# Kernel optimization log

Measured on AMD Instinct MI355X. Metric: run time of the kernel, lower is better.

Reference implementation:

```python
import jax, jax.numpy as jnp
import numpy as np

NUM_HEADS = 8
SCALE = 25.0
SIM_THRESH = 0.75


def setup_inputs() -> dict:
    key = jax.random.key(0)
    k1, k2, k3, k4 = jax.random.split(key, 4)
    B, N, C = 1, 2048, 1024
    x_cls = jax.random.normal(k1, (B, N, C), jnp.float32)
    cls_score = jax.random.uniform(k2, (N,), jnp.float32)
    fg_score = jax.random.uniform(k3, (N,), jnp.float32)
    W_qkv = jax.random.normal(k4, (3 * C, C), jnp.float32) * 0.02
    return {"x_cls": x_cls, "cls_score": cls_score, "fg_score": fg_score, "W_qkv": W_qkv}


def reference(x_cls, cls_score, fg_score, W_qkv):
    B, N, C = x_cls.shape
    H = NUM_HEADS
    hd = C // H
    # qkv projection (Linear without bias): [B,N,3C] -> [3,B,H,N,hd]
    qkv = (x_cls @ W_qkv.T).reshape(B, N, 3, H, hd).transpose(2, 0, 3, 1, 4)
    q, k, v = qkv[0], qkv[1], qkv[2]
    # cosine normalization
    qn = q / jnp.linalg.norm(q, axis=-1, keepdims=True)
    kn = k / jnp.linalg.norm(k, axis=-1, keepdims=True)
    vn = v / jnp.linalg.norm(v, axis=-1, keepdims=True)
    # cls_score broadcast to [1,1,1,N] (columns); fg_score is unused downstream
    cs = cls_score.reshape(1, 1, 1, N)
    # raw v-v similarity map [B,H,N,N]
    attn_cls_raw = vn @ jnp.swapaxes(vn, -2, -1)
    # use_mask=True path: mask[i,j] = cls_score[j] > cls_score[i] - 0.1
    cs_mask = (cs > jnp.swapaxes(cs, -2, -1) - 0.1).astype(x_cls.dtype)
    # scaled, score-weighted, masked attention; dropout p=0 is identity
    attn = jax.nn.softmax((qn @ jnp.swapaxes(kn, -2, -1)) * SCALE * cs * cs_mask, axis=-1)
    x = jnp.swapaxes(attn @ v, 1, 2).reshape(B, N, C)
    x_ori = jnp.swapaxes(v, 1, 2).reshape(B, N, C)
    x_out = jnp.concatenate([x, x_ori], axis=-1)  # [B,N,2C]
    # ave=True branch: head-averaged similarity + second softmax, masked renorm
    sim_raw = attn_cls_raw.sum(axis=1)[0] / H  # [N,N]
    sim_mask = (sim_raw > SIM_THRESH).astype(x_cls.dtype)
    sim_attn = attn.sum(axis=1)[0] / H
    sim_round2 = jax.nn.softmax(sim_attn, axis=-1)
    masked = sim_mask * sim_round2
    sim_round2 = masked / jnp.sum(masked, axis=-1, keepdims=True)
    return (x_out, sim_round2)
```

## Files before the change

### kernel.cpp

```cpp
#include <hip/hip_runtime.h>
#include <cstdint>

typedef unsigned short u16;
typedef __attribute__((ext_vector_type(8))) short short8;
typedef __attribute__((ext_vector_type(4))) short short4v;
typedef __attribute__((ext_vector_type(4))) float f32x4;

#define NTOK 2048
#define CDIM 1024
#define C3   3072
#define NH   8
#define HD   128

__device__ __forceinline__ float bf2f(u16 u) {
    return __uint_as_float(((unsigned)u) << 16);
}
__device__ __forceinline__ u16 f2bf(float f) {
    unsigned u = __float_as_uint(f);
    u += 0x7fffu + ((u >> 16) & 1u);
    return (u16)(u >> 16);
}
__device__ __forceinline__ void gld_lds16(const u16* g, u16* l) {
    __builtin_amdgcn_global_load_lds(
        (__attribute__((address_space(1))) void*)(u16*)g,
        (__attribute__((address_space(3))) void*)l, 16, 0, 0);
}

__global__ __launch_bounds__(256) void k_cast(const float* __restrict__ x,
                                              const float* __restrict__ w,
                                              u16* __restrict__ xb,
                                              u16* __restrict__ wb) {
    int t = blockIdx.x * blockDim.x + threadIdx.x;
    int stride = gridDim.x * blockDim.x;
    for (int i = t; i < (NTOK * CDIM) / 4; i += stride) {
        float4 v = ((const float4*)x)[i];
        ushort4 o;
        o.x = f2bf(v.x); o.y = f2bf(v.y); o.z = f2bf(v.z); o.w = f2bf(v.w);
        ((ushort4*)xb)[i] = o;
    }
    for (int i = t; i < (C3 * CDIM) / 4; i += stride) {
        float4 v = ((const float4*)w)[i];
        ushort4 o;
        o.x = f2bf(v.x); o.y = f2bf(v.y); o.z = f2bf(v.z); o.w = f2bf(v.w);
        ((ushort4*)wb)[i] = o;
    }
}

__global__ __launch_bounds__(256) void k_qkvn(const u16* __restrict__ A,
                                              const u16* __restrict__ B,
                                              u16* __restrict__ Qn,
                                              u16* __restrict__ Kn,
                                              u16* __restrict__ Vn,
                                              u16* __restrict__ Vt,
                                              float* __restrict__ out) {
    __shared__ u16 lds[128 * 136];
    __shared__ float rowssq[128][2];
    u16* As = lds;
    u16* Bs = lds + 128 * 64;
    const int tid = threadIdx.x;
    const int lane = tid & 63;
    const int wid = tid >> 6;
    const int wm = wid >> 1, wn = wid & 1;
    const int q = lane >> 4, l16 = lane & 15;
    const int s = blockIdx.x;
    const int which = s >> 3, h = s & 7;
    const int m0 = blockIdx.y * 128, n0 = s * 128;

    f32x4 zero4 = {0.f, 0.f, 0.f, 0.f};
    f32x4 acc[4][4];
#pragma unroll
    for (int i = 0; i < 4; i++)
#pragma unroll
        for (int j = 0; j < 4; j++) acc[i][j] = zero4;

    const u16* aP[4];
    const u16* bP[4];
#pragma unroll
    for (int t = 0; t < 4; t++) {
        int sl = tid + t * 256;
        int r = sl >> 3, c = (sl & 7) * 8;
        aP[t] = &A[(long long)(m0 + r) * CDIM + c];
        bP[t] = &B[(long long)(n0 + r) * CDIM + c];
    }

    for (int k0 = 0; k0 < CDIM; k0 += 64) {
        __syncthreads();
#pragma unroll
        for (int t = 0; t < 4; t++) {
            int sl = tid + t * 256;
            gld_lds16(aP[t] + k0, &As[sl * 8]);
            gld_lds16(bP[t] + k0, &Bs[sl * 8]);
        }
        __syncthreads();
#pragma unroll
        for (int ks = 0; ks < 2; ks++) {
            short8 af[4], bfr[4];
#pragma unroll
            for (int tm = 0; tm < 4; tm++)
                af[tm] = *(const short8*)&As[(wm * 64 + tm * 16 + l16) * 64 + ks * 32 + q * 8];
#pragma unroll
            for (int tn = 0; tn < 4; tn++)
                bfr[tn] = *(const short8*)&Bs[(wn * 64 + tn * 16 + l16) * 64 + ks * 32 + q * 8];
#pragma unroll
            for (int tm = 0; tm < 4; tm++)
#pragma unroll
                for (int tn = 0; tn < 4; tn++)
                    acc[tm][tn] = __builtin_amdgcn_mfma_f32_16x16x32_bf16(
                        af[tm], bfr[tn], acc[tm][tn], 0, 0, 0);
        }
    }

    __syncthreads();
#pragma unroll
    for (int tm = 0; tm < 4; tm++)
#pragma unroll
        for (int r = 0; r < 4; r++) {
            float p = 0.f;
#pragma unroll
            for (int tn = 0; tn < 4; tn++) p += acc[tm][tn][r] * acc[tm][tn][r];
            p += __shfl_xor(p, 1);
            p += __shfl_xor(p, 2);
            p += __shfl_xor(p, 4);
            p += __shfl_xor(p, 8);
            if (l16 == 0) rowssq[wm * 64 + tm * 16 + q * 4 + r][wn] = p;
        }
    __syncthreads();
    float rinv[4][4];
#pragma unroll
    for (int tm = 0; tm < 4; tm++)
#pragma unroll
        for (int r = 0; r < 4; r++) {
            int rl = wm * 64 + tm * 16 + q * 4 + r;
            rinv[tm][r] = rsqrtf(rowssq[rl][0] + rowssq[rl][1]);
        }
    u16* dstBase = (which == 0 ? Qn : which == 1 ? Kn : Vn);
#pragma unroll
    for (int tm = 0; tm < 4; tm++)
#pragma unroll
        for (int tn = 0; tn < 4; tn++)
#pragma unroll
            for (int r = 0; r < 4; r++) {
                int rl = wm * 64 + tm * 16 + q * 4 + r;
                int d = wn * 64 + tn * 16 + l16;
                dstBase[(long long)(m0 + rl) * CDIM + h * HD + d] =
                    f2bf(acc[tm][tn][r] * rinv[tm][r]);
            }
    if (which == 2) {
#pragma unroll
        for (int tm = 0; tm < 4; tm++)
#pragma unroll
            for (int tn = 0; tn < 4; tn++)
#pragma unroll
                for (int r = 0; r < 4; r++) {
                    int rl = wm * 64 + tm * 16 + q * 4 + r;
                    int d = wn * 64 + tn * 16 + l16;
                    float v = acc[tm][tn][r];
                    out[(long long)(m0 + rl) * 2048 + 1024 + h * HD + d] = v;
                    lds[rl * 136 + d] = f2bf(v);
                }
        __syncthreads();
#pragma unroll
        for (int p = 0; p < 2; p++) {
            int drow = p * 64 + (tid >> 2);
            int nc = (tid & 3) * 32;
            u16 buf[32];
#pragma unroll
            for (int i = 0; i < 32; i++) buf[i] = lds[(nc + i) * 136 + drow];
            u16* dst = &Vt[(long long)(h * HD + drow) * NTOK + m0 + nc];
            *(short8*)&dst[0] = *(short8*)&buf[0];
            *(short8*)&dst[8] = *(short8*)&buf[8];
            *(short8*)&dst[16] = *(short8*)&buf[16];
            *(short8*)&dst[24] = *(short8*)&buf[24];
        }
    }
}

__global__ __launch_bounds__(256) void k_gemm_mask(const u16* __restrict__ A,
                                                   const u16* __restrict__ B,
                                                   unsigned char* __restrict__ Cv,
                                                   int K, int lda, int ldb, int ldc,
                                                   float scale) {
    if (blockIdx.x > blockIdx.y) return;
    __shared__ u16 As[128 * 64];
    __shared__ u16 Bs[128 * 64];
    __shared__ __attribute__((aligned(16))) unsigned char Tm[128][144];
    __shared__ __attribute__((aligned(16))) unsigned char Tt[128][144];
    const int tid = threadIdx.x;
    const int lane = tid & 63;
    const int wid = tid >> 6;
    const int wm = wid >> 1, wn = wid & 1;
    const int q = lane >> 4, l16 = lane & 15;
    const int m0 = blockIdx.y * 128, n0 = blockIdx.x * 128;

    f32x4 zero4 = {0.f, 0.f, 0.f, 0.f};
    f32x4 acc[4][4];
#pragma unroll
    for (int i = 0; i < 4; i++)
#pragma unroll
        for (int j = 0; j < 4; j++) acc[i][j] = zero4;

    const u16* aP[4];
    const u16* bP[4];
#pragma unroll
    for (int t = 0; t < 4; t++) {
        int s = tid + t * 256;
        int r = s >> 3, c = (s & 7) * 8;
        aP[t] = &A[(long long)(m0 + r) * lda + c];
        bP[t] = &B[(long long)(n0 + r) * ldb + c];
    }

    for (int k0 = 0; k0 < K; k0 += 64) {
        __syncthreads();
#pragma unroll
        for (int t = 0; t < 4; t++) {
            int s = tid + t * 256;
            gld_lds16(aP[t] + k0, &As[s * 8]);
            gld_lds16(bP[t] + k0, &Bs[s * 8]);
        }
        __syncthreads();
#pragma unroll
        for (int ks = 0; ks < 2; ks++) {
            short8 af[4], bfr[4];
#pragma unroll
            for (int tm = 0; tm < 4; tm++)
                af[tm] = *(const short8*)&As[(wm * 64 + tm * 16 + l16) * 64 + ks * 32 + q * 8];
#pragma unroll
            for (int tn = 0; tn < 4; tn++)
                bfr[tn] = *(const short8*)&Bs[(wn * 64 + tn * 16 + l16) * 64 + ks * 32 + q * 8];
#pragma unroll
            for (int tm = 0; tm < 4; tm++)
#pragma unroll
                for (int tn = 0; tn < 4; tn++)
                    acc[tm][tn] = __builtin_amdgcn_mfma_f32_16x16x32_bf16(
                        af[tm], bfr[tn], acc[tm][tn], 0, 0, 0);
        }
    }

#pragma unroll
    for (int tm = 0; tm < 4; tm++)
#pragma unroll
        for (int tn = 0; tn < 4; tn++) {
            int col = wn * 64 + tn * 16 + l16;
            int rowbase = wm * 64 + tm * 16 + q * 4;
            unsigned pack = 0;
#pragma unroll
            for (int r = 0; r < 4; r++) {
                unsigned char b = (acc[tm][tn][r] * scale > 0.75f) ? 1 : 0;
                Tm[rowbase + r][col] = b;
                pack |= ((unsigned)b) << (8 * r);
            }
            *(unsigned*)&Tt[col][rowbase] = pack;
        }
    __syncthreads();
    {
        int row = tid >> 1, half = (tid & 1) * 64;
        const short8* sm = (const short8*)&Tm[row][half];
        short8* dm = (short8*)&Cv[(long long)(m0 + row) * ldc + n0 + half];
        dm[0] = sm[0]; dm[1] = sm[1]; dm[2] = sm[2]; dm[3] = sm[3];
        const short8* st = (const short8*)&Tt[row][half];
        short8* dt = (short8*)&Cv[(long long)(n0 + row) * ldc + m0 + half];
        dt[0] = st[0]; dt[1] = st[1]; dt[2] = st[2]; dt[3] = st[3];
    }
}

__global__ __launch_bounds__(256, 4) void k_attn8(const u16* __restrict__ Qn,
                                                  const u16* __restrict__ Kn,
                                                  const u16* __restrict__ Vt,
                                                  const float* __restrict__ cls,
                                                  u16* __restrict__ P,
                                                  float* __restrict__ Spart,
                                                  u16* __restrict__ Xpart) {
    __shared__ u16 Kf[2][8192];
    __shared__ u16 Vf[2][8192];
    __shared__ u16 Et[4096];
    const int h = blockIdx.z;
    const int jc = blockIdx.y;
    const int i0 = blockIdx.x * 64;
    const int jbase = jc * 512;
    const int tid = threadIdx.x, lane = tid & 63, wid = tid >> 6;
    const int q = lane >> 4, l16 = lane & 15;
    const int wm = wid >> 1, wn = wid & 1;

    short8 af[2][4];
#pragma unroll
    for (int m = 0; m < 2; m++)
#pragma unroll
        for (int kt = 0; kt < 4; kt++)
            af[m][kt] = *(const short8*)&Qn[(long long)(i0 + wm * 32 + m * 16 + l16) * CDIM +
                                            h * HD + kt * 32 + q * 8];
    float cls_i[2][4];
#pragma unroll
    for (int m = 0; m < 2; m++)
#pragma unroll
        for (int r = 0; r < 4; r++)
            cls_i[m][r] = cls[i0 + wm * 32 + m * 16 + q * 4 + r] - 0.1f;

    const u16* ksrc[4];
    const u16* vsrc[4];
#pragma unroll
    for (int t = 0; t < 4; t++) {
        int g = wid * 4 + t;
        int tn = g >> 2, kt = g & 3;
        ksrc[t] = &Kn[(long long)(jbase + tn * 16 + l16) * CDIM + h * HD + kt * 32 + q * 8];
        int n = g >> 1, ks = g & 1;
        vsrc[t] = &Vt[(long long)(h * HD + n * 16 + l16) * NTOK + jbase + (ks * 4 + q) * 8];
    }

    f32x4 zero4 = {0.f, 0.f, 0.f, 0.f};
    f32x4 pv[2][4];
#pragma unroll
    for (int m = 0; m < 2; m++)
#pragma unroll
        for (int n = 0; n < 4; n++) pv[m][n] = zero4;
    float sums[2][4] = {{0.f, 0.f, 0.f, 0.f}, {0.f, 0.f, 0.f, 0.f}};

#pragma unroll
    for (int t = 0; t < 4; t++) {
        int g = wid * 4 + t;
        gld_lds16(ksrc[t], &Kf[0][(g * 64 + lane) * 8]);
        gld_lds16(vsrc[t], &Vf[0][(g * 64 + lane) * 8]);
        ksrc[t] += 64 * CDIM;
        vsrc[t] += 64;
    }

    for (int jt = 0; jt < 8; ++jt) {
        const int j0 = jbase + jt * 64;
        const int cur = jt & 1;
        u16* Kc = Kf[cur];
        u16* Vc = Vf[cur];
        if (jt == 0)
            asm volatile("s_waitcnt vmcnt(0)" ::: "memory");
        else
            asm volatile("s_waitcnt vmcnt(2)" ::: "memory");
        __builtin_amdgcn_s_barrier();
        asm volatile("" ::: "memory");
        if (jt < 7) {
            u16* Kx = Kf[cur ^ 1];
            u16* Vx = Vf[cur ^ 1];
#pragma unroll
            for (int t = 0; t < 4; t++) {
                int g = wid * 4 + t;
                gld_lds16(ksrc[t], &Kx[(g * 64 + lane) * 8]);
                gld_lds16(vsrc[t], &Vx[(g * 64 + lane) * 8]);
                ksrc[t] += 64 * CDIM;
                vsrc[t] += 64;
            }
        }
#pragma unroll
        for (int tn = 0; tn < 2; tn++) {
            int tng = wn * 2 + tn;
            short8 bfr[4];
#pragma unroll
            for (int kt = 0; kt < 4; kt++)
                bfr[kt] = *(const short8*)&Kc[((tng * 4 + kt) * 64 + lane) * 8];
            int j = j0 + tng * 16 + l16;
            float cj = cls[j];
            float sc = 25.f * cj;
#pragma unroll
            for (int m = 0; m < 2; m++) {
                f32x4 acc = zero4;
#pragma unroll
                for (int kt = 0; kt < 4; kt++)
                    acc = __builtin_amdgcn_mfma_f32_16x16x32_bf16(af[m][kt], bfr[kt],
                                                                  acc, 0, 0, 0);
                int ibase = wm * 32 + m * 16 + q * 4;
#pragma unroll
                for (int r = 0; r < 4; r++) {
                    float mk = (cj > cls_i[m][r]) ? 1.f : 0.f;
                    float e = __expf(acc[r] * sc * mk);
                    sums[m][r] += e;
                    int il = ibase + r;
                    int jl = tng * 16 + l16;
                    Et[il * 64 + ((((jl >> 3) ^ (il & 7)) << 3) | (jl & 7))] = f2bf(e);
                }
            }
        }
        asm volatile("s_waitcnt lgkmcnt(0)" ::: "memory");
        __builtin_amdgcn_s_barrier();
        asm volatile("" ::: "memory");
        {
            int il = tid >> 2, c = tid & 3;
            int x = il & 7;
            short8 e0 = *(const short8*)&Et[il * 64 + (((2 * c) ^ x) << 3)];
            short8 e1 = *(const short8*)&Et[il * 64 + (((2 * c + 1) ^ x) << 3)];
            u16* dst = &P[((long long)(h * NTOK + i0 + il)) * NTOK + j0 + c * 16];
            *(short8*)&dst[0] = e0;
            *(short8*)&dst[8] = e1;
        }
#pragma unroll
        for (int ks = 0; ks < 2; ks++) {
            short8 a2[2];
#pragma unroll
            for (int m2 = 0; m2 < 2; m2++) {
                int il = wm * 32 + m2 * 16 + l16;
                int ch = ks * 4 + q;
                a2[m2] = *(const short8*)&Et[il * 64 + ((ch ^ (il & 7)) << 3)];
            }
#pragma unroll
            for (int n2 = 0; n2 < 4; n2++) {
                short8 b2 = *(const short8*)&Vf[cur][(((wn * 4 + n2) * 2 + ks) * 64 + lane) * 8];
#pragma unroll
                for (int m2 = 0; m2 < 2; m2++)
                    pv[m2][n2] = __builtin_amdgcn_mfma_f32_16x16x32_bf16(
                        a2[m2], b2, pv[m2][n2], 0, 0, 0);
            }
        }
        (void)Vc;
    }
#pragma unroll
    for (int m = 0; m < 2; m++)
#pragma unroll
        for (int r = 0; r < 4; r++) {
            float s = sums[m][r];
            s += __shfl_xor(s, 1);
            s += __shfl_xor(s, 2);
            s += __shfl_xor(s, 4);
            s += __shfl_xor(s, 8);
            if (l16 == 0)
                Spart[((wn * 4 + jc) * NH + h) * NTOK + i0 + wm * 32 + m * 16 + q * 4 + r] = s;
        }
    u16* Xp = Xpart + (long long)jc * NTOK * CDIM;
#pragma unroll
    for (int m2 = 0; m2 < 2; m2++)
#pragma unroll
        for (int n2 = 0; n2 < 4; n2++)
#pragma unroll
            for (int r = 0; r < 4; r++) {
                int i = i0 + wm * 32 + m2 * 16 + q * 4 + r;
                int d = wn * 64 + n2 * 16 + l16;
                Xp[(long long)i * CDIM + h * HD + d] = f2bf(pv[m2][n2][r]);
            }
}

__global__ __launch_bounds__(256) void k_epi(const u16* __restrict__ Xpart,
                                             const float* __restrict__ Spart,
                                             const u16* __restrict__ P,
                                             const unsigned char* __restrict__ mask,
                                             float* __restrict__ out,
                                             float* __restrict__ out2) {
    __shared__ float red[256];
    __shared__ float sArr[NH];
    const int i = blockIdx.x;
    const int t = threadIdx.x;
    if (t < NH) {
        float s = 0.f;
#pragma unroll
        for (int g = 0; g < 8; g++) s += Spart[(g * NH + t) * NTOK + i];
        sArr[t] = s;
    }
    __syncthreads();
    {
        int c = t * 4;
        int h = c >> 7;
        float acc[4] = {0.f, 0.f, 0.f, 0.f};
#pragma unroll
        for (int jc = 0; jc < 4; jc++) {
            short4v v = *(const short4v*)&Xpart[(long long)jc * NTOK * CDIM +
                                                (long long)i * CDIM + c];
#pragma unroll
            for (int k = 0; k < 4; k++) acc[k] += bf2f((u16)v[k]);
        }
        float invs = 1.f / sArr[h];
        float4 o;
        o.x = acc[0] * invs; o.y = acc[1] * invs; o.z = acc[2] * invs; o.w = acc[3] * invs;
        *(float4*)&out[(long long)i * 2048 + c] = o;
    }
    float invS[NH];
#pragma unroll
    for (int h = 0; h < NH; h++) invS[h] = 1.f / (8.f * sArr[h]);
    const int c0 = t * 8;
    float a[8] = {0.f, 0.f, 0.f, 0.f, 0.f, 0.f, 0.f, 0.f};
#pragma unroll
    for (int h = 0; h < NH; h++) {
        short8 p = *(const short8*)&P[((long long)h * NTOK + i) * NTOK + c0];
#pragma unroll
        for (int k = 0; k < 8; k++) a[k] += bf2f((u16)p[k]) * invS[h];
    }
    const unsigned char* mrow = mask + (long long)i * NTOK + c0;
    float e[8];
    unsigned char mk[8];
    float part = 0.f;
#pragma unroll
    for (int k = 0; k < 8; k++) {
        e[k] = __expf(a[k]);
        mk[k] = mrow[k];
        if (mk[k]) part += e[k];
    }
    red[t] = part;
    __syncthreads();
    for (int s = 128; s > 0; s >>= 1) {
        if (t < s) red[t] += red[t + s];
        __syncthreads();
    }
    float invT = 1.f / red[0];
    float o[8];
#pragma unroll
    for (int k = 0; k < 8; k++) o[k] = mk[k] ? e[k] * invT : 0.f;
    float4 o0, o1;
    o0.x = o[0]; o0.y = o[1]; o0.z = o[2]; o0.w = o[3];
    o1.x = o[4]; o1.y = o[5]; o1.z = o[6]; o1.w = o[7];
    float* dst = out2 + (long long)i * NTOK + c0;
    *(float4*)dst = o0;
    *(float4*)(dst + 4) = o1;
}

extern "C" void kernel_launch(void* const* d_in, const int* in_sizes, int n_in,
                              void* d_out, int out_size, void* d_ws,
                              size_t ws_size, hipStream_t stream) {
    (void)in_sizes; (void)n_in; (void)out_size; (void)ws_size;
    const float* x = (const float*)d_in[0];
    const float* cls = (const float*)d_in[1];
    const float* Wq = (const float*)d_in[3];
    float* out = (float*)d_out;
    char* ws = (char*)d_ws;

    u16* Xb = (u16*)(ws + 0);
    u16* Wb = (u16*)(ws + 4194304);
    u16* Xpart = (u16*)(ws + 0);
    float* Spart = (float*)(ws + 16777216);
    u16* Qn = (u16*)(ws + 23068672);
    u16* Kn = (u16*)(ws + 27262976);
    u16* Vn = (u16*)(ws + 31457280);
    u16* Vt = (u16*)(ws + 35651584);
    unsigned char* mask = (unsigned char*)(ws + 39845888);
    u16* P = (u16*)(ws + 44040192);

    k_cast<<<1024, 256, 0, stream>>>(x, Wq, Xb, Wb);

    k_qkvn<<<dim3(24, 16), 256, 0, stream>>>(Xb, Wb, Qn, Kn, Vn, Vt, out);

    k_gemm_mask<<<dim3(16, 16), 256, 0, stream>>>(
        Vn, Vn, mask, CDIM, CDIM, CDIM, NTOK, 0.125f);

    k_attn8<<<dim3(32, 4, NH), 256, 0, stream>>>(Qn, Kn, Vt, cls, P, Spart, Xpart);

    k_epi<<<NTOK, 256, 0, stream>>>(Xpart, Spart, P, mask, out,
                                    out + (long long)NTOK * 2048);
}
```

Measured before the change: 210.4 us.

## Double attention row tile to 128 per block for K/V reuse

The attention kernel now covers 128 query rows per block instead of 64. Each wave handles four 16-row MFMA tiles, so every K and V tile staged in LDS feeds twice as many rows, halving global K/V traffic per output. The column cls scores are now loaded once before the barrier, and the vmcnt wait is adjusted to match. The cost is more registers and LDS per block, a lower launch-bounds occupancy hint (2 instead of 4), and half as many blocks (512).

Result: faster. 201.7 us (-4.1%).

```diff
diff --git a/kernel.cpp b/kernel.cpp
--- a/kernel.cpp
+++ b/kernel.cpp
@@ -263,7 +263,7 @@
     }
 }
 
-__global__ __launch_bounds__(256, 4) void k_attn8(const u16* __restrict__ Qn,
+__global__ __launch_bounds__(256, 2) void k_attn9(const u16* __restrict__ Qn,
                                                   const u16* __restrict__ Kn,
                                                   const u16* __restrict__ Vt,
                                                   const float* __restrict__ cls,
@@ -272,28 +272,28 @@
                                                   u16* __restrict__ Xpart) {
     __shared__ u16 Kf[2][8192];
     __shared__ u16 Vf[2][8192];
-    __shared__ u16 Et[4096];
+    __shared__ u16 Et[8192];
     const int h = blockIdx.z;
     const int jc = blockIdx.y;
-    const int i0 = blockIdx.x * 64;
+    const int i0 = blockIdx.x * 128;
     const int jbase = jc * 512;
     const int tid = threadIdx.x, lane = tid & 63, wid = tid >> 6;
     const int q = lane >> 4, l16 = lane & 15;
     const int wm = wid >> 1, wn = wid & 1;
 
-    short8 af[2][4];
-#pragma unroll
-    for (int m = 0; m < 2; m++)
+    short8 af[4][4];
+#pragma unroll
+    for (int m = 0; m < 4; m++)
 #pragma unroll
         for (int kt = 0; kt < 4; kt++)
-            af[m][kt] = *(const short8*)&Qn[(long long)(i0 + wm * 32 + m * 16 + l16) * CDIM +
+            af[m][kt] = *(const short8*)&Qn[(long long)(i0 + wm * 64 + m * 16 + l16) * CDIM +
                                             h * HD + kt * 32 + q * 8];
-    float cls_i[2][4];
-#pragma unroll
-    for (int m = 0; m < 2; m++)
+    float cls_i[4][4];
+#pragma unroll
+    for (int m = 0; m < 4; m++)
 #pragma unroll
         for (int r = 0; r < 4; r++)
-            cls_i[m][r] = cls[i0 + wm * 32 + m * 16 + q * 4 + r] - 0.1f;
+            cls_i[m][r] = cls[i0 + wm * 64 + m * 16 + q * 4 + r] - 0.1f;
 
     const u16* ksrc[4];
     const u16* vsrc[4];
@@ -307,12 +307,16 @@
     }
 
     f32x4 zero4 = {0.f, 0.f, 0.f, 0.f};
-    f32x4 pv[2][4];
-#pragma unroll
-    for (int m = 0; m < 2; m++)
+    f32x4 pv[4][4];
+#pragma unroll
+    for (int m = 0; m < 4; m++)
 #pragma unroll
         for (int n = 0; n < 4; n++) pv[m][n] = zero4;
-    float sums[2][4] = {{0.f, 0.f, 0.f, 0.f}, {0.f, 0.f, 0.f, 0.f}};
+    float sums[4][4];
+#pragma unroll
+    for (int m = 0; m < 4; m++)
+#pragma unroll
+        for (int r = 0; r < 4; r++) sums[m][r] = 0.f;
 
 #pragma unroll
     for (int t = 0; t < 4; t++) {
@@ -327,11 +331,14 @@
         const int j0 = jbase + jt * 64;
         const int cur = jt & 1;
         u16* Kc = Kf[cur];
-        u16* Vc = Vf[cur];
         if (jt == 0)
             asm volatile("s_waitcnt vmcnt(0)" ::: "memory");
         else
-            asm volatile("s_waitcnt vmcnt(2)" ::: "memory");
+            asm volatile("s_waitcnt vmcnt(4)" ::: "memory");
+        float cjv[2];
+        cjv[0] = cls[j0 + (wn * 2 + 0) * 16 + l16];
+        cjv[1] = cls[j0 + (wn * 2 + 1) * 16 + l16];
+        asm volatile("" ::: "memory");
         __builtin_amdgcn_s_barrier();
         asm volatile("" ::: "memory");
         if (jt < 7) {
@@ -353,17 +360,16 @@
 #pragma unroll
             for (int kt = 0; kt < 4; kt++)
                 bfr[kt] = *(const short8*)&Kc[((tng * 4 + kt) * 64 + lane) * 8];
-            int j = j0 + tng * 16 + l16;
-            float cj = cls[j];
+            float cj = cjv[tn];
             float sc = 25.f * cj;
 #pragma unroll
-            for (int m = 0; m < 2; m++) {
+            for (int m = 0; m < 4; m++) {
                 f32x4 acc = zero4;
 #pragma unroll
                 for (int kt = 0; kt < 4; kt++)
                     acc = __builtin_amdgcn_mfma_f32_16x16x32_bf16(af[m][kt], bfr[kt],
                                                                   acc, 0, 0, 0);
-                int ibase = wm * 32 + m * 16 + q * 4;
+                int ibase = wm * 64 + m * 16 + q * 4;
 #pragma unroll
                 for (int r = 0; r < 4; r++) {
                     float mk = (cj > cls_i[m][r]) ? 1.f : 0.f;
@@ -379,20 +385,24 @@
         __builtin_amdgcn_s_barrier();
         asm volatile("" ::: "memory");
         {
-            int il = tid >> 2, c = tid & 3;
+            int il = tid >> 1, c4 = (tid & 1) * 4;
             int x = il & 7;
-            short8 e0 = *(const short8*)&Et[il * 64 + (((2 * c) ^ x) << 3)];
-            short8 e1 = *(const short8*)&Et[il * 64 + (((2 * c + 1) ^ x) << 3)];
-            u16* dst = &P[((long long)(h * NTOK + i0 + il)) * NTOK + j0 + c * 16];
+            short8 e0 = *(const short8*)&Et[il * 64 + (((c4 + 0) ^ x) << 3)];
+            short8 e1 = *(const short8*)&Et[il * 64 + (((c4 + 1) ^ x) << 3)];
+            short8 e2 = *(const short8*)&Et[il * 64 + (((c4 + 2) ^ x) << 3)];
+            short8 e3 = *(const short8*)&Et[il * 64 + (((c4 + 3) ^ x) << 3)];
+            u16* dst = &P[((long long)(h * NTOK + i0 + il)) * NTOK + j0 + c4 * 8];
             *(short8*)&dst[0] = e0;
             *(short8*)&dst[8] = e1;
+            *(short8*)&dst[16] = e2;
+            *(short8*)&dst[24] = e3;
         }
 #pragma unroll
         for (int ks = 0; ks < 2; ks++) {
-            short8 a2[2];
-#pragma unroll
-            for (int m2 = 0; m2 < 2; m2++) {
-                int il = wm * 32 + m2 * 16 + l16;
+            short8 a2[4];
+#pragma unroll
+            for (int m2 = 0; m2 < 4; m2++) {
+                int il = wm * 64 + m2 * 16 + l16;
                 int ch = ks * 4 + q;
                 a2[m2] = *(const short8*)&Et[il * 64 + ((ch ^ (il & 7)) << 3)];
             }
@@ -400,15 +410,14 @@
             for (int n2 = 0; n2 < 4; n2++) {
                 short8 b2 = *(const short8*)&Vf[cur][(((wn * 4 + n2) * 2 + ks) * 64 + lane) * 8];
 #pragma unroll
-                for (int m2 = 0; m2 < 2; m2++)
+                for (int m2 = 0; m2 < 4; m2++)
                     pv[m2][n2] = __builtin_amdgcn_mfma_f32_16x16x32_bf16(
                         a2[m2], b2, pv[m2][n2], 0, 0, 0);
             }
         }
-        (void)Vc;
-    }
-#pragma unroll
-    for (int m = 0; m < 2; m++)
+    }
+#pragma unroll
+    for (int m = 0; m < 4; m++)
 #pragma unroll
         for (int r = 0; r < 4; r++) {
             float s = sums[m][r];
@@ -417,16 +426,16 @@
             s += __shfl_xor(s, 4);
             s += __shfl_xor(s, 8);
             if (l16 == 0)
-                Spart[((wn * 4 + jc) * NH + h) * NTOK + i0 + wm * 32 + m * 16 + q * 4 + r] = s;
+                Spart[((wn * 4 + jc) * NH + h) * NTOK + i0 + wm * 64 + m * 16 + q * 4 + r] = s;
         }
     u16* Xp = Xpart + (long long)jc * NTOK * CDIM;
 #pragma unroll
-    for (int m2 = 0; m2 < 2; m2++)
+    for (int m2 = 0; m2 < 4; m2++)
 #pragma unroll
         for (int n2 = 0; n2 < 4; n2++)
 #pragma unroll
             for (int r = 0; r < 4; r++) {
-                int i = i0 + wm * 32 + m2 * 16 + q * 4 + r;
+                int i = i0 + wm * 64 + m2 * 16 + q * 4 + r;
                 int d = wn * 64 + n2 * 16 + l16;
                 Xp[(long long)i * CDIM + h * HD + d] = f2bf(pv[m2][n2][r]);
             }
@@ -532,7 +541,7 @@
     k_gemm_mask<<<dim3(16, 16), 256, 0, stream>>>(
         Vn, Vn, mask, CDIM, CDIM, CDIM, NTOK, 0.125f);
 
-    k_attn8<<<dim3(32, 4, NH), 256, 0, stream>>>(Qn, Kn, Vt, cls, P, Spart, Xpart);
+    k_attn9<<<dim3(16, 4, NH), 256, 0, stream>>>(Qn, Kn, Vt, cls, P, Spart, Xpart);
 
     k_epi<<<NTOK, 256, 0, stream>>>(Xpart, Spart, P, mask, out,
                                     out + (long long)NTOK * 2048);
```
